# Optimization experiments

Hardware: AMD Instinct MI355X
Metric: run time of the kernel (lower is better)

## Reference

```python
import jax, jax.numpy as jnp
import numpy as np

NUM_EXPERTS = 64


def setup_inputs() -> dict:
    key = jax.random.key(0)
    k1, k2 = jax.random.split(key)
    x = jax.random.normal(k1, (4, 4096, 2048), dtype=jnp.float32)
    # nn.Linear default init scale ~ 1/sqrt(dim); exact init irrelevant for correctness
    gate_w = jax.random.normal(k2, (NUM_EXPERTS, 2048), dtype=jnp.float32) * (1.0 / np.sqrt(2048.0))
    expert_bias = jnp.zeros((NUM_EXPERTS,), dtype=jnp.float32)
    return {"x": x, "gate_w": gate_w, "expert_bias": expert_bias, "top_k": 8}


def reference(x, gate_w, expert_bias, top_k):
    # x: [B, S, D]; gate_w: [E, D]; expert_bias: [E]
    B, S, D = x.shape
    x_flat = x.reshape(-1, D)                                  # [T, D], T = B*S
    logits = jnp.einsum('td,ed->te', x_flat, gate_w) + expert_bias  # [T, E]
    top_k_logits, top_k_indices = jax.lax.top_k(logits, top_k)      # [T, K]
    top_k_weights = jax.nn.softmax(top_k_logits, axis=-1)           # [T, K]
    # training-mode load counting (scatter_add over expert ids)
    expert_counts = jax.ops.segment_sum(
        jnp.ones((B * S * top_k,), dtype=jnp.float32),
        top_k_indices.reshape(-1),
        num_segments=NUM_EXPERTS,
    )                                                               # [E]
    return top_k_indices, top_k_weights, expert_counts
```

## Files before the change

### kernel.cpp

```cpp
#include <hip/hip_runtime.h>
#include <math.h>

#define T_TOKENS 16384
#define D_DIM    2048
#define E_EXP    64
#define TOPK     8
#define NS       8
#define NCH      (D_DIM / NS / 32)

typedef __attribute__((ext_vector_type(8))) short bf16x8;
typedef __attribute__((ext_vector_type(4))) float f32x4;

__device__ __forceinline__ unsigned short bf16rne(float f) {
  unsigned u = __builtin_bit_cast(unsigned, f);
  unsigned r = u + 0x7fffu + ((u >> 16) & 1u);
  return (unsigned short)(r >> 16);
}
__device__ __forceinline__ float bf16f(unsigned short h) {
  return __builtin_bit_cast(float, (unsigned)h << 16);
}

__device__ __forceinline__ void split8(const float4 v0, const float4 v1,
                                       bf16x8& hi, bf16x8& lo) {
  const float xs[8] = {v0.x, v0.y, v0.z, v0.w, v1.x, v1.y, v1.z, v1.w};
  #pragma unroll
  for (int j = 0; j < 8; ++j) {
    unsigned short h = bf16rne(xs[j]);
    hi[j] = (short)h;
    lo[j] = (short)bf16rne(xs[j] - bf16f(h));
  }
}

__global__ __launch_bounds__(256) void convert_g_kernel(
    const float* __restrict__ gw, unsigned short* __restrict__ ph,
    unsigned short* __restrict__ pl, float* __restrict__ counts_zero)
{
  const int id = blockIdx.x * 256 + threadIdx.x;
  if (blockIdx.x == 0 && threadIdx.x < E_EXP) counts_zero[threadIdx.x] = 0.0f;

  const int e  = id & 63;
  const int kq = (id >> 6) & 3;
  const int c  = id >> 8;
  const float* gp = &gw[(size_t)e * D_DIM + c * 32 + kq * 8];
  float4 v0 = *(const float4*)&gp[0];
  float4 v1 = *(const float4*)&gp[4];
  bf16x8 hi, lo;
  split8(v0, v1, hi, lo);
  *(bf16x8*)&ph[(size_t)id * 8] = hi;
  *(bf16x8*)&pl[(size_t)id * 8] = lo;
}

__global__ __launch_bounds__(256, 4) void moe_logits_kernel(
    const float* __restrict__ x, const unsigned short* __restrict__ ph,
    const unsigned short* __restrict__ pl, float* __restrict__ part)
{
  const int tid  = threadIdx.x;
  const int wave = tid >> 6;
  const int lane = tid & 63;
  const int l15  = lane & 15;
  const int quad = lane >> 4;
  const int ks   = blockIdx.y;
  const int k0   = ks * (D_DIM / NS);
  const int tokw = blockIdx.x * 64 + wave * 16;

  f32x4 acc[4];
  #pragma unroll
  for (int et = 0; et < 4; ++et) acc[et] = (f32x4){0.f, 0.f, 0.f, 0.f};

  const float* xp = &x[(size_t)(tokw + l15) * D_DIM + k0 + quad * 8];
  const unsigned short* bh_p = &ph[(((size_t)(k0 >> 5) * 4 + quad) * 64 + l15) * 8];
  const unsigned short* bl_p = &pl[(((size_t)(k0 >> 5) * 4 + quad) * 64 + l15) * 8];

  #pragma unroll 2
  for (int c = 0; c < NCH; ++c) {
    float4 v0 = *(const float4*)&xp[0];
    float4 v1 = *(const float4*)&xp[4];
    xp += 32;

    bf16x8 ah, al;
    split8(v0, v1, ah, al);

    #pragma unroll
    for (int et = 0; et < 4; ++et) {
      bf16x8 bh = *(const bf16x8*)&bh_p[et * 128];
      bf16x8 bl = *(const bf16x8*)&bl_p[et * 128];
      acc[et] = __builtin_amdgcn_mfma_f32_16x16x32_bf16(ah, bh, acc[et], 0, 0, 0);
      acc[et] = __builtin_amdgcn_mfma_f32_16x16x32_bf16(al, bh, acc[et], 0, 0, 0);
      acc[et] = __builtin_amdgcn_mfma_f32_16x16x32_bf16(ah, bl, acc[et], 0, 0, 0);
    }
    bh_p += 2048;
    bl_p += 2048;
  }

  #pragma unroll
  for (int et = 0; et < 4; ++et) {
    #pragma unroll
    for (int r = 0; r < 4; ++r) {
      const size_t t = (size_t)tokw + quad * 4 + r;
      part[((size_t)ks * T_TOKENS + t) * E_EXP + et * 16 + l15] = acc[et][r];
    }
  }
}

__global__ __launch_bounds__(64) void topk_kernel(
    const float* __restrict__ part, const float* __restrict__ bias,
    float* __restrict__ out)
{
  __shared__ unsigned hist[E_EXP];
  const int tid = threadIdx.x;
  const int t = blockIdx.x * 64 + tid;
  hist[tid] = 0;
  __syncthreads();

  float l[E_EXP];
  #pragma unroll
  for (int j = 0; j < E_EXP / 4; ++j) {
    float4 b = *(const float4*)&bias[j * 4];
    l[4*j] = b.x; l[4*j+1] = b.y; l[4*j+2] = b.z; l[4*j+3] = b.w;
  }
  #pragma unroll 1
  for (int ks = 0; ks < NS; ++ks) {
    const float4* p = (const float4*)&part[((size_t)ks * T_TOKENS + t) * E_EXP];
    #pragma unroll
    for (int j = 0; j < E_EXP / 4; ++j) {
      float4 v = p[j];
      l[4*j] += v.x; l[4*j+1] += v.y; l[4*j+2] += v.z; l[4*j+3] += v.w;
    }
  }

  float tv[TOPK]; int tix[TOPK];
  unsigned long long used = 0ull;
  #pragma unroll
  for (int k = 0; k < TOPK; ++k) {
    float best = -INFINITY; int bi = 0;
    #pragma unroll
    for (int j = 0; j < E_EXP; ++j) {
      bool ok = (((used >> j) & 1ull) == 0ull) && (l[j] > best);
      best = ok ? l[j] : best;
      bi   = ok ? j : bi;
    }
    tv[k] = best; tix[k] = bi;
    used |= (1ull << bi);
  }

  float m = tv[0], s = 0.0f, w[TOPK];
  #pragma unroll
  for (int k = 0; k < TOPK; ++k) { w[k] = expf(tv[k] - m); s += w[k]; }
  float inv = 1.0f / s;

  #pragma unroll
  for (int k = 0; k < TOPK; ++k) {
    out[(size_t)t * TOPK + k] = (float)tix[k];
    out[(size_t)T_TOKENS * TOPK + (size_t)t * TOPK + k] = w[k] * inv;
  }

  #pragma unroll
  for (int k = 0; k < TOPK; ++k) atomicAdd(&hist[tix[k]], 1u);
  __syncthreads();
  atomicAdd(&out[2 * (size_t)T_TOKENS * TOPK + tid], (float)hist[tid]);
}

extern "C" void kernel_launch(void* const* d_in, const int* in_sizes, int n_in,
                              void* d_out, int out_size, void* d_ws, size_t ws_size,
                              hipStream_t stream) {
  const float* x    = (const float*)d_in[0];
  const float* gw   = (const float*)d_in[1];
  const float* bias = (const float*)d_in[2];
  float* out  = (float*)d_out;

  float* part = (float*)d_ws;
  const size_t part_elems = (size_t)NS * T_TOKENS * E_EXP;
  unsigned short* ph = (unsigned short*)((char*)d_ws + part_elems * sizeof(float));
  unsigned short* pl = ph + (size_t)E_EXP * D_DIM;

  convert_g_kernel<<<dim3(E_EXP * D_DIM / 8 / 256), dim3(256), 0, stream>>>(
      gw, ph, pl, out + 2 * (size_t)T_TOKENS * TOPK);
  moe_logits_kernel<<<dim3(T_TOKENS / 64, NS), dim3(256), 0, stream>>>(
      x, ph, pl, part);
  topk_kernel<<<dim3(T_TOKENS / 64), dim3(64), 0, stream>>>(part, bias, out);
}
```

Measured before the change: 241.4 us.

## Stage x tiles through padded LDS with register prefetch and halve K-splits

The logits kernel now loads each 64-token x chunk with coalesced float4 reads into a padded, transposed LDS tile. It prefetches the next chunk into registers while the current one is converted and fed to the MFMAs. The number of K splits drops from 8 to 4, which halves the partial-sum traffic written by this kernel and read back by topk. The cost is two barriers per chunk, strided LDS reads, and half as many blocks for the GPU to schedule.

```diff
diff --git a/kernel.cpp b/kernel.cpp
--- a/kernel.cpp
+++ b/kernel.cpp
@@ -5,8 +5,11 @@
 #define D_DIM    2048
 #define E_EXP    64
 #define TOPK     8
-#define NS       8
-#define NCH      (D_DIM / NS / 32)
+#define NS       4
+#define KC       32
+#define NCH      (D_DIM / NS / KC)
+#define TT       64
+#define XS       65
 
 typedef __attribute__((ext_vector_type(8))) short bf16x8;
 typedef __attribute__((ext_vector_type(4))) float f32x4;
@@ -18,17 +21,6 @@
 }
 __device__ __forceinline__ float bf16f(unsigned short h) {
   return __builtin_bit_cast(float, (unsigned)h << 16);
-}
-
-__device__ __forceinline__ void split8(const float4 v0, const float4 v1,
-                                       bf16x8& hi, bf16x8& lo) {
-  const float xs[8] = {v0.x, v0.y, v0.z, v0.w, v1.x, v1.y, v1.z, v1.w};
-  #pragma unroll
-  for (int j = 0; j < 8; ++j) {
-    unsigned short h = bf16rne(xs[j]);
-    hi[j] = (short)h;
-    lo[j] = (short)bf16rne(xs[j] - bf16f(h));
-  }
 }
 
 __global__ __launch_bounds__(256) void convert_g_kernel(
@@ -44,8 +36,14 @@
   const float* gp = &gw[(size_t)e * D_DIM + c * 32 + kq * 8];
   float4 v0 = *(const float4*)&gp[0];
   float4 v1 = *(const float4*)&gp[4];
+  const float xs[8] = {v0.x, v0.y, v0.z, v0.w, v1.x, v1.y, v1.z, v1.w};
   bf16x8 hi, lo;
-  split8(v0, v1, hi, lo);
+  #pragma unroll
+  for (int j = 0; j < 8; ++j) {
+    unsigned short h = bf16rne(xs[j]);
+    hi[j] = (short)h;
+    lo[j] = (short)bf16rne(xs[j] - bf16f(h));
+  }
   *(bf16x8*)&ph[(size_t)id * 8] = hi;
   *(bf16x8*)&pl[(size_t)id * 8] = lo;
 }
@@ -54,6 +52,8 @@
     const float* __restrict__ x, const unsigned short* __restrict__ ph,
     const unsigned short* __restrict__ pl, float* __restrict__ part)
 {
+  __shared__ float xl[KC * XS];
+
   const int tid  = threadIdx.x;
   const int wave = tid >> 6;
   const int lane = tid & 63;
@@ -61,35 +61,66 @@
   const int quad = lane >> 4;
   const int ks   = blockIdx.y;
   const int k0   = ks * (D_DIM / NS);
-  const int tokw = blockIdx.x * 64 + wave * 16;
+  const int tok0 = blockIdx.x * TT;
+  const int tokw = tok0 + wave * 16;
+
+  const int sr  = tid >> 3;
+  const int sc4 = tid & 7;
 
   f32x4 acc[4];
   #pragma unroll
   for (int et = 0; et < 4; ++et) acc[et] = (f32x4){0.f, 0.f, 0.f, 0.f};
 
-  const float* xp = &x[(size_t)(tokw + l15) * D_DIM + k0 + quad * 8];
   const unsigned short* bh_p = &ph[(((size_t)(k0 >> 5) * 4 + quad) * 64 + l15) * 8];
   const unsigned short* bl_p = &pl[(((size_t)(k0 >> 5) * 4 + quad) * 64 + l15) * 8];
 
-  #pragma unroll 2
+  const float* xg0 = &x[(size_t)(tok0 + sr)      * D_DIM + k0 + sc4 * 4];
+  const float* xg1 = &x[(size_t)(tok0 + sr + 32) * D_DIM + k0 + sc4 * 4];
+  float4 p0 = *(const float4*)xg0;
+  float4 p1 = *(const float4*)xg1;
+
+  #pragma unroll 1
   for (int c = 0; c < NCH; ++c) {
-    float4 v0 = *(const float4*)&xp[0];
-    float4 v1 = *(const float4*)&xp[4];
-    xp += 32;
-
+    __syncthreads();
+    {
+      float* d0 = &xl[(sc4 * 4) * XS + sr];
+      float* d1 = &xl[(sc4 * 4) * XS + sr + 32];
+      d0[0*XS] = p0.x; d0[1*XS] = p0.y; d0[2*XS] = p0.z; d0[3*XS] = p0.w;
+      d1[0*XS] = p1.x; d1[1*XS] = p1.y; d1[2*XS] = p1.z; d1[3*XS] = p1.w;
+    }
+    __syncthreads();
+
+    if (c + 1 < NCH) {
+      p0 = *(const float4*)(xg0 + (c + 1) * KC);
+      p1 = *(const float4*)(xg1 + (c + 1) * KC);
+    }
+
+    const unsigned short* ch = bh_p + (size_t)c * 2048;
+    const unsigned short* cl = bl_p + (size_t)c * 2048;
+    bf16x8 bh[4], bl[4];
+    #pragma unroll
+    for (int et = 0; et < 4; ++et) {
+      bh[et] = *(const bf16x8*)&ch[et * 128];
+      bl[et] = *(const bf16x8*)&cl[et * 128];
+    }
+
+    float xr[8];
+    #pragma unroll
+    for (int j = 0; j < 8; ++j) xr[j] = xl[(quad * 8 + j) * XS + wave * 16 + l15];
     bf16x8 ah, al;
-    split8(v0, v1, ah, al);
+    #pragma unroll
+    for (int j = 0; j < 8; ++j) {
+      unsigned short h = bf16rne(xr[j]);
+      ah[j] = (short)h;
+      al[j] = (short)bf16rne(xr[j] - bf16f(h));
+    }
 
     #pragma unroll
     for (int et = 0; et < 4; ++et) {
-      bf16x8 bh = *(const bf16x8*)&bh_p[et * 128];
-      bf16x8 bl = *(const bf16x8*)&bl_p[et * 128];
-      acc[et] = __builtin_amdgcn_mfma_f32_16x16x32_bf16(ah, bh, acc[et], 0, 0, 0);
-      acc[et] = __builtin_amdgcn_mfma_f32_16x16x32_bf16(al, bh, acc[et], 0, 0, 0);
-      acc[et] = __builtin_amdgcn_mfma_f32_16x16x32_bf16(ah, bl, acc[et], 0, 0, 0);
-    }
-    bh_p += 2048;
-    bl_p += 2048;
+      acc[et] = __builtin_amdgcn_mfma_f32_16x16x32_bf16(ah, bh[et], acc[et], 0, 0, 0);
+      acc[et] = __builtin_amdgcn_mfma_f32_16x16x32_bf16(al, bh[et], acc[et], 0, 0, 0);
+      acc[et] = __builtin_amdgcn_mfma_f32_16x16x32_bf16(ah, bl[et], acc[et], 0, 0, 0);
+    }
   }
 
   #pragma unroll
@@ -175,7 +206,7 @@
 
   convert_g_kernel<<<dim3(E_EXP * D_DIM / 8 / 256), dim3(256), 0, stream>>>(
       gw, ph, pl, out + 2 * (size_t)T_TOKENS * TOPK);
-  moe_logits_kernel<<<dim3(T_TOKENS / 64, NS), dim3(256), 0, stream>>>(
+  moe_logits_kernel<<<dim3(T_TOKENS / TT, NS), dim3(256), 0, stream>>>(
       x, ph, pl, part);
   topk_kernel<<<dim3(T_TOKENS / 64), dim3(64), 0, stream>>>(part, bias, out);
 }
```

After: 230.6 us. 4.5% less time.
